# Kernel tuning notes

Hardware: AMD Instinct MI355X
Metric: run time of the kernel (lower is better)

Reference implementation:

```python
import jax, jax.numpy as jnp
import numpy as np

N_HEADS = 32
N_KV = 8
GROUPS = 4
D_HEAD = 64
ROPE_BASE = 10000.0


def _rope_tables(seq_len):
    # inv_freq over even dims, emb = [freqs, freqs] along last axis (torch cat([outer]*2))
    inv_freq = 1.0 / (ROPE_BASE ** (jnp.arange(0, D_HEAD, 2, dtype=jnp.float32) / D_HEAD))
    t = jnp.arange(seq_len, dtype=jnp.float32)
    freqs = jnp.outer(t, inv_freq)                      # [S, D_HEAD/2]
    emb = jnp.concatenate([freqs, freqs], axis=-1)      # [S, D_HEAD]
    return jnp.cos(emb), jnp.sin(emb)


def _rotate_half(x):
    h = x.shape[-1] // 2
    return jnp.concatenate([-x[..., h:], x[..., :h]], axis=-1)


def setup_inputs() -> dict:
    key = jax.random.key(0)
    ks = jax.random.split(key, 5)
    B, S, D = 4, 2048, 2048
    s = 0.02
    return {
        "x": jax.random.normal(ks[0], (B, S, D), dtype=jnp.float32),
        "Wq": jax.random.normal(ks[1], (D, D), dtype=jnp.float32) * s,
        "Wk": jax.random.normal(ks[2], (N_KV * D_HEAD, D), dtype=jnp.float32) * s,
        "Wv": jax.random.normal(ks[3], (N_KV * D_HEAD, D), dtype=jnp.float32) * s,
        "Wo": jax.random.normal(ks[4], (D, D), dtype=jnp.float32) * s,
        "temperature": jnp.float32(1.0),
    }


def reference(x, Wq, Wk, Wv, Wo, temperature):
    B, S, D = x.shape
    # QKV projections (torch Linear: x @ W.T)
    Q = jnp.einsum('bsd,ed->bse', x, Wq).reshape(B, S, N_HEADS, D_HEAD).transpose(0, 2, 1, 3)
    K = jnp.einsum('bsd,ed->bse', x, Wk).reshape(B, S, N_KV, D_HEAD).transpose(0, 2, 1, 3)
    V = jnp.einsum('bsd,ed->bse', x, Wv).reshape(B, S, N_KV, D_HEAD).transpose(0, 2, 1, 3)

    # RoPE (offset=0, no past_kv)
    cos, sin = _rope_tables(S)          # [S, D_HEAD]
    cos = cos[None, None]
    sin = sin[None, None]
    Q = Q * cos + _rotate_half(Q) * sin
    K = K * cos + _rotate_half(K) * sin

    kv_cache = (K, V)  # pre-expansion cache, as in original

    # GQA expand: each kv head repeated GROUPS times along head axis
    Ke = jnp.repeat(K, GROUPS, axis=1)  # [B, N_HEADS, S, D_HEAD]
    Ve = jnp.repeat(V, GROUPS, axis=1)

    # scale uses .item() in torch -> constant w.r.t. autograd
    scale = (D_HEAD ** -0.5) / jnp.maximum(jnp.abs(temperature), 1e-6)
    scale = jax.lax.stop_gradient(scale)

    scores = jnp.einsum('bhqd,bhkd->bhqk', Q, Ke) * scale
    causal = jnp.tril(jnp.ones((S, S), dtype=bool))
    scores = jnp.where(causal[None, None], scores, jnp.finfo(scores.dtype).min)
    attn = jax.nn.softmax(scores, axis=-1)
    out = jnp.einsum('bhqk,bhkd->bhqd', attn, Ve)       # [B, H, S, D_HEAD]

    out = out.transpose(0, 2, 1, 3).reshape(B, S, D)
    y = jnp.einsum('bsd,ed->bse', out, Wo)
    return (y, kv_cache[0], kv_cache[1])
```

## Files before the change

kernel.cpp:

```cpp
#include <hip/hip_runtime.h>

#define S_LEN  2048
#define DMODEL 2048
#define NH     32
#define NKV    8
#define DH     64

typedef _Float16 h8   __attribute__((ext_vector_type(8)));
typedef _Float16 h4   __attribute__((ext_vector_type(4)));
typedef float    f32x4 __attribute__((ext_vector_type(4)));

__device__ __forceinline__ void load_lds16(const _Float16* g, _Float16* l) {
  typedef const __attribute__((address_space(1))) unsigned int* gp_t;
  typedef __attribute__((address_space(3))) unsigned int* lp_t;
  __builtin_amdgcn_global_load_lds((gp_t)g, (lp_t)l, 16, 0, 0);
}

#define N8_X  2097152
#define N8_WQ 524288
#define N8_WK 131072
#define N8_WV 131072
#define N8_WO 524288
#define N8_ALL (N8_X + N8_WQ + N8_WK + N8_WV + N8_WO)
__global__ void cvt_all(const float* __restrict__ x, const float* __restrict__ wq,
                        const float* __restrict__ wk, const float* __restrict__ wv,
                        const float* __restrict__ wo, _Float16* __restrict__ dst) {
  int stride = gridDim.x * blockDim.x;
  for (int i = blockIdx.x * blockDim.x + threadIdx.x; i < N8_ALL; i += stride) {
    const float* s;
    int off;
    if (i < N8_X) { s = x; off = i; }
    else if (i < N8_X + N8_WQ) { s = wq; off = i - N8_X; }
    else if (i < N8_X + N8_WQ + N8_WK) { s = wk; off = i - (N8_X + N8_WQ); }
    else if (i < N8_X + N8_WQ + N8_WK + N8_WV) { s = wv; off = i - (N8_X + N8_WQ + N8_WK); }
    else { s = wo; off = i - (N8_X + N8_WQ + N8_WK + N8_WV); }
    float4 a = ((const float4*)s)[2 * off];
    float4 b = ((const float4*)s)[2 * off + 1];
    h8 v = {(_Float16)a.x, (_Float16)a.y, (_Float16)a.z, (_Float16)a.w,
            (_Float16)b.x, (_Float16)b.y, (_Float16)b.z, (_Float16)b.w};
    ((h8*)dst)[i] = v;
  }
}

__global__ void rope_table_k(float2* __restrict__ tab) {
  int i = blockIdx.x * blockDim.x + threadIdx.x;
  int s = i >> 5, d = i & 31;
  float invf = (float)exp2(-(double)d * 0.4152410118609203);
  float angf = (float)s * invf;
  double a = (double)angf;
  const double twopi = 6.283185307179586476925287;
  a -= floor(a / twopi) * twopi;
  tab[i] = make_float2((float)cos(a), (float)sin(a));
}

template <int MODE>
__global__ __launch_bounds__(512, 2) void gemm256(
    const _Float16* __restrict__ A, const _Float16* __restrict__ Bm,
    _Float16* __restrict__ qH, _Float16* __restrict__ kH, float* __restrict__ kF,
    _Float16* __restrict__ vH, float* __restrict__ vF, float* __restrict__ yF,
    const float2* __restrict__ rtab, const float* __restrict__ tptr) {
  __shared__ __align__(16) _Float16 lA[2][256 * 64];
  __shared__ __align__(16) _Float16 lB[2][256 * 64];
  const int Kd = 2048;
  int t = threadIdx.x;
  int w = t >> 6, lane = t & 63;
  int n0 = blockIdx.x * 256, m0 = blockIdx.y * 256;
  int wr = w >> 2, wc = w & 3;
  int lq = lane & 15, hi = lane >> 4;

  int swz = ((lane & 7) ^ (lane >> 3)) * 8;
  const _Float16* pA = A + (size_t)(m0 + w * 32 + (lane >> 3)) * Kd + swz;
  const _Float16* pB = Bm + (size_t)(n0 + w * 32 + (lane >> 3)) * Kd + swz;
  int dRow = (w * 32) * 64;

  f32x4 z4 = {0.f, 0.f, 0.f, 0.f};
  f32x4 acc[8][4];
#pragma unroll
  for (int i = 0; i < 8; i++)
#pragma unroll
    for (int j = 0; j < 4; j++) acc[i][j] = z4;

#pragma unroll
  for (int i = 0; i < 4; i++)
    load_lds16(pB + (size_t)(i * 8) * Kd, &lB[0][dRow + i * 8 * 64]);
#pragma unroll
  for (int i = 0; i < 4; i++)
    load_lds16(pA + (size_t)(i * 8) * Kd, &lA[0][dRow + i * 8 * 64]);

  const int NT = Kd / 64;
  for (int tt = 0; tt < NT; tt++) {
    int cur = tt & 1, nxt = cur ^ 1;

    asm volatile("s_waitcnt vmcnt(4)" ::: "memory");
    __builtin_amdgcn_s_barrier();

    if (tt + 1 < NT) {
      int k0n = (tt + 1) * 64;
#pragma unroll
      for (int i = 0; i < 4; i++)
        load_lds16(pB + (size_t)(i * 8) * Kd + k0n, &lB[nxt][dRow + i * 8 * 64]);
#pragma unroll
      for (int i = 0; i < 4; i++)
        load_lds16(pA + (size_t)(i * 8) * Kd + k0n, &lA[nxt][dRow + i * 8 * 64]);
    }

    h8 bf[4][2];
#pragma unroll
    for (int j = 0; j < 4; j++)
#pragma unroll
      for (int s = 0; s < 2; s++)
        bf[j][s] = *(const h8*)&lB[cur][(wc * 64 + j * 16 + lq) * 64 + (((s * 4 + hi) ^ (lq & 7)) * 8)];

    if (tt + 1 < NT) {
      asm volatile("s_waitcnt vmcnt(8)" ::: "memory");
    } else {
      asm volatile("s_waitcnt vmcnt(0)" ::: "memory");
    }
    __builtin_amdgcn_s_barrier();

#pragma unroll
    for (int p = 0; p < 4; p++) {
      h8 af[2][2];
#pragma unroll
      for (int di = 0; di < 2; di++)
#pragma unroll
        for (int s = 0; s < 2; s++)
          af[di][s] = *(const h8*)&lA[cur][(wr * 128 + (p * 2 + di) * 16 + lq) * 64 + (((s * 4 + hi) ^ (lq & 7)) * 8)];
      __builtin_amdgcn_s_setprio(1);
#pragma unroll
      for (int s = 0; s < 2; s++)
#pragma unroll
        for (int di = 0; di < 2; di++)
#pragma unroll
          for (int j = 0; j < 4; j++)
            acc[p * 2 + di][j] = __builtin_amdgcn_mfma_f32_16x16x32_f16(af[di][s], bf[j][s], acc[p * 2 + di][j], 0, 0, 0);
      __builtin_amdgcn_s_setprio(0);
    }
  }

  if (MODE == 3) {
#pragma unroll
    for (int ci = 0; ci < 4; ci++) {
      int col = n0 + wc * 64 + ci * 16 + lq;
#pragma unroll
      for (int i = 0; i < 8; i++)
#pragma unroll
        for (int r = 0; r < 4; r++) {
          int m = m0 + wr * 128 + i * 16 + hi * 4 + r;
          yF[(size_t)m * DMODEL + col] = acc[i][ci][r];
        }
    }
  } else {
    int base64 = n0 + wc * 64;
    if (base64 < 2048) {
      float qsc = 0.125f / fmaxf(fabsf(tptr[0]), 1e-6f) * 1.4426950408889634f;
      int head = base64 >> 6;
#pragma unroll
      for (int ci = 0; ci < 2; ci++) {
        int dlo = ci * 16 + lq;
#pragma unroll
        for (int i = 0; i < 8; i++)
#pragma unroll
          for (int r = 0; r < 4; r++) {
            int m = m0 + wr * 128 + i * 16 + hi * 4 + r;
            int b = m >> 11, s = m & 2047;
            float2 cs = rtab[s * 32 + dlo];
            float lo = acc[i][ci][r], hv = acc[i][ci + 2][r];
            float olo = (lo * cs.x - hv * cs.y) * qsc;
            float ohi = (hv * cs.x + lo * cs.y) * qsc;
            size_t base = ((size_t)(b * NH + head) * S_LEN + s) * DH;
            qH[base + dlo] = (_Float16)olo;
            qH[base + dlo + 32] = (_Float16)ohi;
          }
      }
    } else if (base64 < 2560) {
      int head = (base64 - 2048) >> 6;
#pragma unroll
      for (int ci = 0; ci < 2; ci++) {
        int dlo = ci * 16 + lq;
#pragma unroll
        for (int i = 0; i < 8; i++)
#pragma unroll
          for (int r = 0; r < 4; r++) {
            int m = m0 + wr * 128 + i * 16 + hi * 4 + r;
            int b = m >> 11, s = m & 2047;
            float2 cs = rtab[s * 32 + dlo];
            float lo = acc[i][ci][r], hv = acc[i][ci + 2][r];
            float olo = lo * cs.x - hv * cs.y;
            float ohi = hv * cs.x + lo * cs.y;
            size_t bb = ((size_t)(b * NKV + head) * S_LEN + s) * DH;
            kH[bb + dlo] = (_Float16)olo;
            kH[bb + dlo + 32] = (_Float16)ohi;
            kF[bb + dlo] = olo;
            kF[bb + dlo + 32] = ohi;
          }
      }
    } else {
      int head = (base64 - 2560) >> 6;
#pragma unroll
      for (int ci = 0; ci < 4; ci++) {
        int d = ci * 16 + lq;
#pragma unroll
        for (int i = 0; i < 8; i++)
#pragma unroll
          for (int r = 0; r < 4; r++) {
            int m = m0 + wr * 128 + i * 16 + hi * 4 + r;
            int b = m >> 11, s = m & 2047;
            float v = acc[i][ci][r];
            vH[((size_t)(b * NKV + head) * DH + d) * S_LEN + s] = (_Float16)v;
            vF[((size_t)(b * NKV + head) * S_LEN + s) * DH + d] = v;
          }
      }
    }
  }
}

__global__ __launch_bounds__(256, 3) void attn_fwd(
    const _Float16* __restrict__ Q, const _Float16* __restrict__ K,
    const _Float16* __restrict__ Vt, _Float16* __restrict__ AO) {
  __shared__ __align__(16) _Float16 lP[4][32 * 72];
  __shared__ __align__(16) _Float16 lK[2][64 * 64];
  __shared__ __align__(16) _Float16 lV[2][64 * 64];
  int t = threadIdx.x, w = t >> 6, lane = t & 63;
  int lq = lane & 15, hi = lane >> 4;

  int bh = blockIdx.x * 16 + (blockIdx.y & 15);
  int qb = 15 - (blockIdx.y >> 4);
  int b = bh >> 5, h = bh & 31, g = h >> 2;

  const _Float16* Qp = Q + ((size_t)(b * NH + h) * S_LEN) * DH;
  const _Float16* Kp = K + ((size_t)(b * NKV + g) * S_LEN) * DH;
  const _Float16* Vp = Vt + ((size_t)(b * NKV + g) * DH) * S_LEN;

  f32x4 z4 = {0.f, 0.f, 0.f, 0.f};
  int q0 = qb * 128 + w * 32;

  int swz = ((lane & 7) ^ (lane >> 3)) * 8;
  size_t sko0 = (size_t)(w * 16 + (lane >> 3)) * DH + (size_t)swz;
  size_t svo0 = (size_t)(w * 16 + (lane >> 3)) * S_LEN + (size_t)swz;

  h8 qf[2][2];
#pragma unroll
  for (int cf = 0; cf < 2; cf++)
#pragma unroll
    for (int dc = 0; dc < 2; dc++)
      qf[cf][dc] = *(const h8*)&Qp[(size_t)(q0 + lq + 16 * cf) * DH + dc * 32 + hi * 8];

  f32x4 ot[4][2];
#pragma unroll
  for (int rf = 0; rf < 4; rf++)
#pragma unroll
    for (int cf = 0; cf < 2; cf++) ot[rf][cf] = z4;
  float mrun[2] = {-3e38f, -3e38f};
  float lrun[2] = {0.f, 0.f};

  int NT = 2 * qb + 2;

  load_lds16(Kp + sko0, &lK[0][(w * 16) * 64]);
  load_lds16(Kp + sko0 + (size_t)8 * DH, &lK[0][(w * 16 + 8) * 64]);
  load_lds16(Vp + svo0, &lV[0][(w * 16) * 64]);
  load_lds16(Vp + svo0 + (size_t)8 * S_LEN, &lV[0][(w * 16 + 8) * 64]);

  for (int tk = 0; tk < NT; tk++) {
    int kv0 = tk * 64;

    asm volatile("s_waitcnt vmcnt(0)" ::: "memory");
    __builtin_amdgcn_s_barrier();

    if (tk + 1 < NT) {
      _Float16* nK = &lK[(tk + 1) & 1][0];
      _Float16* nV = &lV[(tk + 1) & 1][0];
      size_t kvn = (size_t)(kv0 + 64);
      load_lds16(Kp + kvn * DH + sko0, nK + (w * 16) * 64);
      load_lds16(Kp + kvn * DH + sko0 + (size_t)8 * DH, nK + (w * 16 + 8) * 64);
      load_lds16(Vp + svo0 + kvn, nV + (w * 16) * 64);
      load_lds16(Vp + svo0 + kvn + (size_t)8 * S_LEN, nV + (w * 16 + 8) * 64);
    }

    f32x4 sc[4][2];
#pragma unroll
    for (int rf = 0; rf < 4; rf++)
#pragma unroll
      for (int cf = 0; cf < 2; cf++) sc[rf][cf] = z4;
    {
      const _Float16* kb = &lK[tk & 1][0];
#pragma unroll
      for (int dc = 0; dc < 2; dc++) {
        h8 kf[4];
#pragma unroll
        for (int rf = 0; rf < 4; rf++)
          kf[rf] = *(const h8*)&kb[(rf * 16 + lq) * 64 + (((dc * 4 + hi) ^ (lq & 7)) * 8)];
#pragma unroll
        for (int rf = 0; rf < 4; rf++)
#pragma unroll
          for (int cf = 0; cf < 2; cf++)
            sc[rf][cf] = __builtin_amdgcn_mfma_f32_16x16x32_f16(kf[rf], qf[cf][dc], sc[rf][cf], 0, 0, 0);
      }
    }

    if (kv0 + 63 > q0) {
#pragma unroll
      for (int rf = 0; rf < 4; rf++)
#pragma unroll
        for (int cf = 0; cf < 2; cf++)
#pragma unroll
          for (int r = 0; r < 4; r++) {
            int kv = kv0 + rf * 16 + hi * 4 + r;
            int q = q0 + lq + 16 * cf;
            if (kv > q) sc[rf][cf][r] = -1e30f;
          }
    }

    float mt[2];
#pragma unroll
    for (int cf = 0; cf < 2; cf++) {
      float m2 = -3e38f;
#pragma unroll
      for (int rf = 0; rf < 4; rf++)
#pragma unroll
        for (int r = 0; r < 4; r++) m2 = fmaxf(m2, sc[rf][cf][r]);
      m2 = fmaxf(m2, __shfl_xor(m2, 16));
      m2 = fmaxf(m2, __shfl_xor(m2, 32));
      mt[cf] = m2;
    }

    bool need = !__all((mt[0] - mrun[0] <= 8.f) && (mt[1] - mrun[1] <= 8.f));
    if (need) {
#pragma unroll
      for (int cf = 0; cf < 2; cf++) {
        float mnew = fmaxf(mrun[cf], mt[cf]);
        float al = __builtin_amdgcn_exp2f(mrun[cf] - mnew);
        mrun[cf] = mnew;
        lrun[cf] *= al;
#pragma unroll
        for (int rf = 0; rf < 4; rf++)
#pragma unroll
          for (int r = 0; r < 4; r++) ot[rf][cf][r] *= al;
      }
    }

    float ls[2] = {0.f, 0.f};
#pragma unroll
    for (int rf = 0; rf < 4; rf++)
#pragma unroll
      for (int cf = 0; cf < 2; cf++)
#pragma unroll
        for (int r = 0; r < 4; r++) {
          float p = __builtin_amdgcn_exp2f(sc[rf][cf][r] - mrun[cf]);
          sc[rf][cf][r] = p;
          ls[cf] += p;
        }
#pragma unroll
    for (int cf = 0; cf < 2; cf++) {
      float s2 = ls[cf];
      s2 += __shfl_xor(s2, 16);
      s2 += __shfl_xor(s2, 32);
      lrun[cf] += s2;
    }

#pragma unroll
    for (int rf = 0; rf < 4; rf++)
#pragma unroll
      for (int cf = 0; cf < 2; cf++) {
        h4 p4;
#pragma unroll
        for (int r = 0; r < 4; r++) p4[r] = (_Float16)sc[rf][cf][r];
        *(h4*)&lP[w][(lq + 16 * cf) * 72 + rf * 16 + hi * 4] = p4;
      }
    asm volatile("s_waitcnt lgkmcnt(0)" ::: "memory");
    __builtin_amdgcn_sched_barrier(0);

    {
      const _Float16* vb = &lV[tk & 1][0];
#pragma unroll
      for (int kvc = 0; kvc < 2; kvc++) {
        h8 vf[4];
#pragma unroll
        for (int rf = 0; rf < 4; rf++)
          vf[rf] = *(const h8*)&vb[(rf * 16 + lq) * 64 + (((kvc * 4 + hi) ^ (lq & 7)) * 8)];
        h8 pb[2];
#pragma unroll
        for (int cf = 0; cf < 2; cf++)
          pb[cf] = *(const h8*)&lP[w][(lq + 16 * cf) * 72 + kvc * 32 + hi * 8];
#pragma unroll
        for (int rf = 0; rf < 4; rf++)
#pragma unroll
          for (int cf = 0; cf < 2; cf++)
            ot[rf][cf] = __builtin_amdgcn_mfma_f32_16x16x32_f16(vf[rf], pb[cf], ot[rf][cf], 0, 0, 0);
      }
    }
  }

#pragma unroll
  for (int cf = 0; cf < 2; cf++) {
    float inv = 1.0f / lrun[cf];
    size_t row = (size_t)b * S_LEN + q0 + lq + 16 * cf;
#pragma unroll
    for (int rf = 0; rf < 4; rf++) {
      h4 o;
#pragma unroll
      for (int r = 0; r < 4; r++) o[r] = (_Float16)(ot[rf][cf][r] * inv);
      *(h4*)&AO[row * DMODEL + h * DH + rf * 16 + hi * 4] = o;
    }
  }
}

extern "C" void kernel_launch(void* const* d_in, const int* in_sizes, int n_in,
                              void* d_out, int out_size, void* d_ws, size_t ws_size,
                              hipStream_t stream) {
  const float* x  = (const float*)d_in[0];
  const float* Wq = (const float*)d_in[1];
  const float* Wk = (const float*)d_in[2];
  const float* Wv = (const float*)d_in[3];
  const float* Wo = (const float*)d_in[4];
  const float* tp = (const float*)d_in[5];

  float* y  = (float*)d_out;
  float* Ko = y + (size_t)16777216;
  float* Vo = Ko + (size_t)4194304;

  _Float16* xh  = (_Float16*)d_ws;
  _Float16* wqh = xh + 16777216;
  _Float16* wkh = wqh + 4194304;
  _Float16* wvh = wkh + 1048576;
  _Float16* woh = wvh + 1048576;
  _Float16* Kh  = woh + 4194304;
  _Float16* Vth = Kh + 4194304;
  float2*   rtab = (float2*)(Vth + 4194304);
  _Float16* AOh = xh;
  _Float16* Qh  = (_Float16*)d_out;
  (void)wkh; (void)wvh;

  cvt_all<<<2048, 256, 0, stream>>>(x, Wq, Wk, Wv, Wo, xh);
  rope_table_k<<<256, 256, 0, stream>>>(rtab);

  gemm256<1><<<dim3(12, 32), 512, 0, stream>>>(xh, wqh, Qh, Kh, Ko, Vth, Vo, nullptr, rtab, tp);
  attn_fwd<<<dim3(8, 256), 256, 0, stream>>>(Qh, Kh, Vth, AOh);
  gemm256<3><<<dim3(8, 32), 512, 0, stream>>>(AOh, woh, nullptr, nullptr, nullptr, nullptr, nullptr, y, rtab, tp);
}
```

Before: 367.4 us.

## Interleave next-tile global-to-LDS loads with per-phase MFMA in GEMM

Rearranges which rows each wave stages into LDS and splits the next k-tile's loads into four chunks. Each chunk is issued inside one of the four MFMA phases, with fine-grained vmcnt waits and extra barriers per phase. The goal is to spread memory traffic across the compute loop and keep MFMA units fed, in the style of a ping-pong schedule. It adds more barriers per k-tile, and the waitcnt bookkeeping is delicate.

```diff
diff --git a/kernel.cpp b/kernel.cpp
--- a/kernel.cpp
+++ b/kernel.cpp
@@ -69,9 +69,15 @@
   int lq = lane & 15, hi = lane >> 4;
 
   int swz = ((lane & 7) ^ (lane >> 3)) * 8;
-  const _Float16* pA = A + (size_t)(m0 + w * 32 + (lane >> 3)) * Kd + swz;
-  const _Float16* pB = Bm + (size_t)(n0 + w * 32 + (lane >> 3)) * Kd + swz;
-  int dRow = (w * 32) * 64;
+  const _Float16* pB = Bm + (size_t)(n0 + 8 * w + (lane >> 3)) * Kd + swz;
+  const _Float16* pA = A + (size_t)(m0 + (w >> 2) * 128 + (w & 3) * 8 + (lane >> 3)) * Kd + swz;
+  int dB = (8 * w) * 64;
+  int dA = ((w >> 2) * 128 + (w & 3) * 8) * 64;
+
+#define STAGE_B(buf, h, j, k0n) \
+  load_lds16(pB + (size_t)(128 * (h) + 64 * (j)) * Kd + (k0n), &lB[buf][dB + (128 * (h) + 64 * (j)) * 64])
+#define STAGE_A(buf, q, k0n) \
+  load_lds16(pA + (size_t)(32 * (q)) * Kd + (k0n), &lA[buf][dA + 32 * (q) * 64])
 
   f32x4 z4 = {0.f, 0.f, 0.f, 0.f};
   f32x4 acc[8][4];
@@ -80,63 +86,67 @@
 #pragma unroll
     for (int j = 0; j < 4; j++) acc[i][j] = z4;
 
-#pragma unroll
-  for (int i = 0; i < 4; i++)
-    load_lds16(pB + (size_t)(i * 8) * Kd, &lB[0][dRow + i * 8 * 64]);
-#pragma unroll
-  for (int i = 0; i < 4; i++)
-    load_lds16(pA + (size_t)(i * 8) * Kd, &lA[0][dRow + i * 8 * 64]);
+  STAGE_B(0, 0, 0, 0); STAGE_B(0, 0, 1, 0);
+  STAGE_B(0, 1, 0, 0); STAGE_B(0, 1, 1, 0);
+  STAGE_A(0, 0, 0); STAGE_A(0, 1, 0); STAGE_A(0, 2, 0); STAGE_A(0, 3, 0);
 
   const int NT = Kd / 64;
   for (int tt = 0; tt < NT; tt++) {
     int cur = tt & 1, nxt = cur ^ 1;
-
-    asm volatile("s_waitcnt vmcnt(4)" ::: "memory");
-    __builtin_amdgcn_s_barrier();
-
-    if (tt + 1 < NT) {
-      int k0n = (tt + 1) * 64;
-#pragma unroll
-      for (int i = 0; i < 4; i++)
-        load_lds16(pB + (size_t)(i * 8) * Kd + k0n, &lB[nxt][dRow + i * 8 * 64]);
-#pragma unroll
-      for (int i = 0; i < 4; i++)
-        load_lds16(pA + (size_t)(i * 8) * Kd + k0n, &lA[nxt][dRow + i * 8 * 64]);
-    }
-
+    int k0n = (tt + 1) * 64;
+    bool more = (tt + 1 < NT);
     h8 bf[4][2];
 #pragma unroll
-    for (int j = 0; j < 4; j++)
+    for (int p = 0; p < 4; p++) {
+      if (p == 0)      asm volatile("s_waitcnt vmcnt(3)" ::: "memory");
+      else if (more) {
+        if (p == 1)      asm volatile("s_waitcnt vmcnt(4)" ::: "memory");
+        else if (p == 2) asm volatile("s_waitcnt vmcnt(5)" ::: "memory");
+        else             asm volatile("s_waitcnt vmcnt(6)" ::: "memory");
+      } else {
+        if (p == 1)      asm volatile("s_waitcnt vmcnt(2)" ::: "memory");
+        else if (p == 2) asm volatile("s_waitcnt vmcnt(1)" ::: "memory");
+        else             asm volatile("s_waitcnt vmcnt(0)" ::: "memory");
+      }
+      asm volatile("s_barrier" ::: "memory");
+
+      if (more) {
+        if (p == 0)      { STAGE_B(nxt, 0, 0, k0n); STAGE_B(nxt, 0, 1, k0n); }
+        else if (p == 1) { STAGE_B(nxt, 1, 0, k0n); STAGE_B(nxt, 1, 1, k0n); }
+        else if (p == 2) { STAGE_A(nxt, 0, k0n); STAGE_A(nxt, 1, k0n); }
+        else             { STAGE_A(nxt, 2, k0n); STAGE_A(nxt, 3, k0n); }
+      }
+
+      if (p == 0) {
+#pragma unroll
+        for (int j = 0; j < 4; j++)
+#pragma unroll
+          for (int s = 0; s < 2; s++)
+            bf[j][s] = *(const h8*)&lB[cur][(wc * 64 + j * 16 + lq) * 64 + (((s * 4 + hi) ^ (lq & 7)) * 8)];
+      }
+      h8 af[2][2];
+#pragma unroll
+      for (int di = 0; di < 2; di++)
+#pragma unroll
+        for (int s = 0; s < 2; s++)
+          af[di][s] = *(const h8*)&lA[cur][(wr * 128 + 32 * p + di * 16 + lq) * 64 + (((s * 4 + hi) ^ (lq & 7)) * 8)];
+
+      asm volatile("s_barrier" ::: "memory");
+      asm volatile("s_waitcnt lgkmcnt(0)" ::: "memory");
+      __builtin_amdgcn_sched_barrier(0);
+      __builtin_amdgcn_s_setprio(1);
 #pragma unroll
       for (int s = 0; s < 2; s++)
-        bf[j][s] = *(const h8*)&lB[cur][(wc * 64 + j * 16 + lq) * 64 + (((s * 4 + hi) ^ (lq & 7)) * 8)];
-
-    if (tt + 1 < NT) {
-      asm volatile("s_waitcnt vmcnt(8)" ::: "memory");
-    } else {
-      asm volatile("s_waitcnt vmcnt(0)" ::: "memory");
-    }
-    __builtin_amdgcn_s_barrier();
-
-#pragma unroll
-    for (int p = 0; p < 4; p++) {
-      h8 af[2][2];
-#pragma unroll
-      for (int di = 0; di < 2; di++)
-#pragma unroll
-        for (int s = 0; s < 2; s++)
-          af[di][s] = *(const h8*)&lA[cur][(wr * 128 + (p * 2 + di) * 16 + lq) * 64 + (((s * 4 + hi) ^ (lq & 7)) * 8)];
-      __builtin_amdgcn_s_setprio(1);
-#pragma unroll
-      for (int s = 0; s < 2; s++)
 #pragma unroll
         for (int di = 0; di < 2; di++)
 #pragma unroll
           for (int j = 0; j < 4; j++)
-            acc[p * 2 + di][j] = __builtin_amdgcn_mfma_f32_16x16x32_f16(af[di][s], bf[j][s], acc[p * 2 + di][j], 0, 0, 0);
+            acc[2 * p + di][j] = __builtin_amdgcn_mfma_f32_16x16x32_f16(af[di][s], bf[j][s], acc[2 * p + di][j], 0, 0, 0);
       __builtin_amdgcn_s_setprio(0);
     }
   }
+#undef STAGE_A
+#undef STAGE_B
 
   if (MODE == 3) {
 #pragma unroll
```

Measured after the change: 424.6 us. 1.16x slower.
